# Optimization experiments

Measured on AMD Instinct MI355X. Metric: run time of the kernel, lower is better.

## Reference

```python
import jax, jax.numpy as jnp
import numpy as np

N, B, C_IN, C, E = 50000, 2, 64, 64, 800000


def _xavier(k, shape):
    bound = np.sqrt(6.0 / (shape[0] + shape[1]))
    return jax.random.uniform(k, shape, jnp.float32, -bound, bound)


def setup_inputs() -> dict:
    key = jax.random.key(0)
    ks = jax.random.split(key, 12)
    X = jax.random.normal(ks[0], (N, B, C_IN), jnp.float32)
    edge_index = jax.random.randint(ks[1], (2, E), 0, N, jnp.int64)
    edge_weight = jax.random.uniform(ks[2], (E,), jnp.float32)
    weight_n = _xavier(ks[3], (C_IN, C))
    weight_e = _xavier(ks[4], (1, C))
    query_w = _xavier(ks[5], (C, C))
    key_w = _xavier(ks[6], (C, C))
    # nn.Linear(3C, 1): store transposed weight [3C, 1] and bias [1]
    lb = 1.0 / np.sqrt(3 * C)
    att_w = jax.random.uniform(ks[7], (3 * C, 1), jnp.float32, -lb, lb)
    att_b = jax.random.uniform(ks[8], (1,), jnp.float32, -lb, lb)
    # nn.Linear(2C, C): store transposed weight [2C, C] and bias [C]
    lb2 = 1.0 / np.sqrt(2 * C)
    out_w = jax.random.uniform(ks[9], (2 * C, C), jnp.float32, -lb2, lb2)
    out_b = jax.random.uniform(ks[10], (C,), jnp.float32, -lb2, lb2)
    return {
        "X": X, "edge_index": edge_index, "edge_weight": edge_weight,
        "weight_n": weight_n, "weight_e": weight_e,
        "query_w": query_w, "key_w": key_w,
        "att_w": att_w, "att_b": att_b,
        "out_w": out_w, "out_b": out_b,
    }


def reference(X, edge_index, edge_weight, weight_n, weight_e,
              query_w, key_w, att_w, att_b, out_w, out_b):
    # node projection: [N, B, C]
    x = jnp.einsum('nbi,ic->nbc', X, weight_n)
    src, dst = edge_index[0], edge_index[1]  # x_j = x[src], x_i = x[dst]
    # edge embedding: [E, C]
    edge_emb = edge_weight[:, None] * weight_e[0][None, :]

    x_j = x[src]  # [E, B, C]
    x_i = x[dst]  # [E, B, C]
    q = jnp.einsum('ebc,cd->ebd', x_j, query_w)
    k = jnp.einsum('ebc,cd->ebd', x_i, key_w)
    # linear_att on concat([q, k, edge_emb]) == split matmul (avoids [E,B,3C] concat)
    wq, wk, we = att_w[:C], att_w[C:2 * C], att_w[2 * C:]
    att_logit = (q @ wq) + (k @ wk) + (edge_emb @ we)[:, None, :] + att_b  # [E, B, 1]
    att = jax.nn.sigmoid(att_logit)
    gate = jax.nn.sigmoid(edge_emb)[:, None, :]  # [E, 1, C]
    msg = att * x_j * gate  # [E, B, C]

    aggr = jax.ops.segment_sum(msg, dst, num_segments=N)  # [N, B, C]

    # linear_out(cat([x, aggr])) as split matmul
    upd = (jnp.einsum('nbc,cd->nbd', x, out_w[:C])
           + jnp.einsum('nbc,cd->nbd', aggr, out_w[C:]) + out_b)
    return x + upd
```

## Files before the change

### kernel.cpp

```cpp
#include <hip/hip_runtime.h>

#define NN 50000
#define BB 2
#define CC 64
#define EE 800000
#define RR (NN * BB)
#define K1BLK (RR / 32)
#define K2BLK (EE / 256)
#define NSCAN ((NN + 255) / 256)

typedef float f4_t __attribute__((ext_vector_type(4)));
typedef float f2_t __attribute__((ext_vector_type(2)));

#define LOG2E 1.44269504f

__device__ __forceinline__ float fsig_(float x) {
    return __builtin_amdgcn_rcpf(1.0f + __builtin_amdgcn_exp2f(x * -LOG2E));
}

__device__ __forceinline__ float bcast_(float v, int d) {
    return __uint_as_float(__builtin_amdgcn_readlane(__float_as_uint(v), d));
}

__global__ void k0_prep(const float* __restrict__ qw, const float* __restrict__ kw,
                        const float* __restrict__ we, const float* __restrict__ aw,
                        const float* __restrict__ wn, const float* __restrict__ ow,
                        float* __restrict__ prep, float* __restrict__ Wc) {
    int t = threadIdx.x;
    if (blockIdx.x == 0) {
        __shared__ float qv_s[64], kv_s[64];
        if (t < 64) {
            float sq = 0.f, sk = 0.f;
            for (int d = 0; d < 64; ++d) {
                sq = fmaf(qw[t * 64 + d], aw[d], sq);
                sk = fmaf(kw[t * 64 + d], aw[64 + d], sk);
            }
            qv_s[t] = sq; kv_s[t] = sk;
            prep[t] = sq; prep[64 + t] = sk;
            prep[320 + t] = -we[t] * LOG2E;
        }
        if (t == 128) {
            float se = 0.f;
            for (int i = 0; i < 64; ++i) se = fmaf(we[i], aw[128 + i], se);
            prep[128] = se;
        }
        __syncthreads();
        if (t < 64) {
            float s = 0.f;
            for (int c = 0; c < 64; ++c) s = fmaf(wn[t * 64 + c], qv_s[c], s);
            prep[192 + t] = s;
        } else if (t < 128) {
            int d = t - 64;
            float s = 0.f;
            for (int c = 0; c < 64; ++c) s = fmaf(wn[d * 64 + c], kv_s[c], s);
            prep[256 + d] = s;
        }
    } else {
        int idx = (blockIdx.x - 1) * 256 + t;
        int d = idx >> 6, c = idx & 63;
        float s = wn[d * 64 + c];
        for (int k = 0; k < 64; ++k) s = fmaf(wn[d * 64 + k], ow[k * 64 + c], s);
        Wc[idx] = s;
    }
}

__global__ void __launch_bounds__(256) k12(
        const float* __restrict__ X, const float* __restrict__ wn,
        const float* __restrict__ Wc, const float* __restrict__ out_b,
        const float* __restrict__ prep, const int* __restrict__ ei,
        float* __restrict__ x2f, float* __restrict__ y0,
        float* __restrict__ dq, float* __restrict__ dk,
        int* __restrict__ count) {
    int t = threadIdx.x;
    if (blockIdx.x < K2BLK) {
        int e = blockIdx.x * 256 + t;
        if (e < EE) atomicAdd(&count[ei[EE + e]], 1);
        return;
    }
    int wave = ((blockIdx.x - K2BLK) * 256 + t) >> 6;
    int lane = t & 63;
    int r0 = wave * 8;
    if (r0 >= RR) return;

    float xin[8];
    #pragma unroll
    for (int j = 0; j < 8; ++j) xin[j] = X[(r0 + j) * 64 + lane];

    float nq_l = prep[192 + lane];
    float nk_l = prep[256 + lane];

    float accx[8], accy[8];
    #pragma unroll
    for (int j = 0; j < 8; ++j) { accx[j] = 0.f; accy[j] = 0.f; }

    #pragma unroll 16
    for (int d = 0; d < 64; ++d) {
        float w0 = wn[d * 64 + lane];
        float wc = Wc[d * 64 + lane];
        #pragma unroll
        for (int j = 0; j < 8; ++j) {
            float s = bcast_(xin[j], d);
            accx[j] = fmaf(s, w0, accx[j]);
            accy[j] = fmaf(s, wc, accy[j]);
        }
    }

    float ob = out_b[lane];
    #pragma unroll
    for (int j = 0; j < 8; ++j) {
        int r = r0 + j;
        y0[r * 64 + lane] = accy[j] + ob;
        x2f[((r >> 1) * 64 + lane) * 2 + (r & 1)] = accx[j];
        float pq = xin[j] * nq_l;
        float pk = xin[j] * nk_l;
        #pragma unroll
        for (int o = 32; o > 0; o >>= 1) {
            pq += __shfl_xor(pq, o, 64);
            pk += __shfl_xor(pk, o, 64);
        }
        if (lane == j) { dq[r] = pq; dk[r] = pk; }
    }
}

__global__ void __launch_bounds__(256) k3a(const int* __restrict__ count,
                                           int* __restrict__ incl,
                                           int* __restrict__ bsum) {
    __shared__ int wsum[4];
    int t = threadIdx.x;
    int i = blockIdx.x * 256 + t;
    int v = (i < NN) ? count[i] : 0;
    int s = v;
    #pragma unroll
    for (int o = 1; o < 64; o <<= 1) {
        int u = __shfl_up(s, o, 64);
        if ((t & 63) >= o) s += u;
    }
    if ((t & 63) == 63) wsum[t >> 6] = s;
    __syncthreads();
    int add = 0;
    for (int w = 0; w < (t >> 6); ++w) add += wsum[w];
    s += add;
    if (i < NN) incl[i] = s;
    if (t == 255) bsum[blockIdx.x] = s;
}

__global__ void __launch_bounds__(256) k3b(const int* __restrict__ bsum,
                                           int* __restrict__ bscan) {
    __shared__ int wsum[4];
    int t = threadIdx.x;
    int v = (t < NSCAN) ? bsum[t] : 0;
    int s = v;
    #pragma unroll
    for (int o = 1; o < 64; o <<= 1) {
        int u = __shfl_up(s, o, 64);
        if ((t & 63) >= o) s += u;
    }
    if ((t & 63) == 63) wsum[t >> 6] = s;
    __syncthreads();
    int add = 0;
    for (int w = 0; w < (t >> 6); ++w) add += wsum[w];
    bscan[t] = s + add;
}

__global__ void __launch_bounds__(256) k3c(const int* __restrict__ count,
                                           const int* __restrict__ incl,
                                           const int* __restrict__ bscan,
                                           int* __restrict__ offs,
                                           int* __restrict__ cursor) {
    int t = threadIdx.x;
    int i = blockIdx.x * 256 + t;
    if (i < NN) {
        int base = blockIdx.x ? bscan[blockIdx.x - 1] : 0;
        int excl = base + incl[i] - count[i];
        offs[i] = excl;
        cursor[i] = excl;
    }
    if (i == 0) offs[NN] = EE;
}

__global__ void k4_scatter(const int* __restrict__ ei, const float* __restrict__ ew,
                           const float2* __restrict__ dq2, const float2* __restrict__ dk2,
                           const float* __restrict__ prep, const float* __restrict__ att_b,
                           int* __restrict__ cursor, f4_t* __restrict__ csr) {
    int e = blockIdx.x * blockDim.x + threadIdx.x;
    if (e >= EE) return;
    int src = ei[e], dst = ei[EE + e];
    float w = ew[e];
    float2 q = dq2[src];
    float2 k = dk2[dst];
    float esc = fmaf(w, prep[128], att_b[0]);
    float a0 = fsig_(q.x + k.x + esc);
    float a1 = fsig_(q.y + k.y + esc);
    int pos = atomicAdd(&cursor[dst], 1);
    f4_t rec = { __int_as_float(src), w, a0, a1 };
    __builtin_nontemporal_store(rec, &csr[pos]);
}

__global__ void __launch_bounds__(256) k5_aggr(
        const int* __restrict__ offs, const f4_t* __restrict__ csr,
        const f2_t* __restrict__ x2, const float* __restrict__ y0,
        const float* __restrict__ prep, const float* __restrict__ ow,
        float* __restrict__ out) {
    __shared__ float w1[4096];
    int t = threadIdx.x;
    #pragma unroll
    for (int j = 0; j < 16; ++j) w1[t + j * 256] = ow[4096 + t + j * 256];
    __syncthreads();

    int n = (blockIdx.x * 256 + t) >> 6;
    int lane = t & 63;
    if (n >= NN) return;

    float weL = prep[320 + lane];
    int s0 = offs[n], s1 = offs[n + 1];
    int cnt = s1 - s0;
    const f4_t* cp = csr + s0;

    float a0 = 0.f, a1 = 0.f;
    int i = 0;
    for (; i + 2 <= cnt; i += 2) {
        f4_t c0 = __builtin_nontemporal_load(cp + i);
        f4_t c1 = __builtin_nontemporal_load(cp + i + 1);
        f2_t xj0 = x2[__float_as_int(c0.x) * 64 + lane];
        f2_t xj1 = x2[__float_as_int(c1.x) * 64 + lane];
        float g0 = __builtin_amdgcn_rcpf(1.0f + __builtin_amdgcn_exp2f(c0.y * weL));
        float g1 = __builtin_amdgcn_rcpf(1.0f + __builtin_amdgcn_exp2f(c1.y * weL));
        a0 = fmaf(c0.z * g0, xj0.x, a0);
        a1 = fmaf(c0.w * g0, xj0.y, a1);
        a0 = fmaf(c1.z * g1, xj1.x, a0);
        a1 = fmaf(c1.w * g1, xj1.y, a1);
    }
    if (i < cnt) {
        f4_t c0 = __builtin_nontemporal_load(cp + i);
        f2_t xj0 = x2[__float_as_int(c0.x) * 64 + lane];
        float g0 = __builtin_amdgcn_rcpf(1.0f + __builtin_amdgcn_exp2f(c0.y * weL));
        a0 = fmaf(c0.z * g0, xj0.x, a0);
        a1 = fmaf(c0.w * g0, xj0.y, a1);
    }

    float o0 = __builtin_nontemporal_load(&y0[(2 * n) * 64 + lane]);
    float o1 = __builtin_nontemporal_load(&y0[(2 * n + 1) * 64 + lane]);
    #pragma unroll 16
    for (int d = 0; d < 64; ++d) {
        float wv = w1[d * 64 + lane];
        o0 = fmaf(bcast_(a0, d), wv, o0);
        o1 = fmaf(bcast_(a1, d), wv, o1);
    }
    __builtin_nontemporal_store(o0, &out[(2 * n) * 64 + lane]);
    __builtin_nontemporal_store(o1, &out[(2 * n + 1) * 64 + lane]);
}

extern "C" void kernel_launch(void* const* d_in, const int* in_sizes, int n_in,
                              void* d_out, int out_size, void* d_ws, size_t ws_size,
                              hipStream_t stream) {
    const float* X        = (const float*)d_in[0];
    const int*   ei       = (const int*)d_in[1];
    const float* ew       = (const float*)d_in[2];
    const float* weight_n = (const float*)d_in[3];
    const float* weight_e = (const float*)d_in[4];
    const float* query_w  = (const float*)d_in[5];
    const float* key_w    = (const float*)d_in[6];
    const float* att_w    = (const float*)d_in[7];
    const float* att_b    = (const float*)d_in[8];
    const float* out_w    = (const float*)d_in[9];
    const float* out_b    = (const float*)d_in[10];
    float* out = (float*)d_out;

    char* ws = (char*)d_ws;
    size_t off = 0;
    auto alloc = [&](size_t bytes) {
        char* p = ws + off;
        off += (bytes + 255) & ~(size_t)255;
        return p;
    };
    float*  x2f    = (float*)alloc(sizeof(float) * NN * CC * BB);
    float*  y0     = (float*)alloc(sizeof(float) * RR * CC);
    float*  dq     = (float*)alloc(sizeof(float) * RR);
    float*  dk     = (float*)alloc(sizeof(float) * RR);
    float*  prep   = (float*)alloc(sizeof(float) * 512);
    float*  Wc     = (float*)alloc(sizeof(float) * 4096);
    int*    count  = (int*)alloc(sizeof(int) * NN);
    int*    incl   = (int*)alloc(sizeof(int) * NN);
    int*    offs   = (int*)alloc(sizeof(int) * (NN + 1));
    int*    cursor = (int*)alloc(sizeof(int) * NN);
    int*    bsum   = (int*)alloc(sizeof(int) * 256);
    int*    bscan  = (int*)alloc(sizeof(int) * 256);
    f4_t*   csr    = (f4_t*)alloc(sizeof(f4_t) * EE);

    hipMemsetAsync(count, 0, sizeof(int) * NN, stream);

    hipLaunchKernelGGL(k0_prep, dim3(17), dim3(256), 0, stream,
                       query_w, key_w, weight_e, att_w, weight_n, out_w, prep, Wc);
    hipLaunchKernelGGL(k12, dim3(K1BLK + K2BLK), dim3(256), 0, stream,
                       X, weight_n, Wc, out_b, prep, ei, x2f, y0, dq, dk, count);
    hipLaunchKernelGGL(k3a, dim3(NSCAN), dim3(256), 0, stream,
                       count, incl, bsum);
    hipLaunchKernelGGL(k3b, dim3(1), dim3(256), 0, stream, bsum, bscan);
    hipLaunchKernelGGL(k3c, dim3(NSCAN), dim3(256), 0, stream,
                       count, incl, bscan, offs, cursor);
    hipLaunchKernelGGL(k4_scatter, dim3(K2BLK), dim3(256), 0, stream,
                       ei, ew, (const float2*)dq, (const float2*)dk, prep, att_b,
                       cursor, csr);
    hipLaunchKernelGGL(k5_aggr, dim3(NN / 4), dim3(256), 0, stream,
                       offs, csr, (const f2_t*)x2f, y0, prep, out_w, out);
}
```

Before: 316.3 us.

## Split aggregation and output matmul into separate kernels, unroll gather by four

The fused aggregate-plus-output-projection kernel is split in two. The aggregation kernel no longer stages a 16KB weight tile in LDS, which should raise occupancy for the latency-bound gather, and it unrolls the edge loop by four. A new k6 kernel does the 64x64 output matmul with each wave handling 8 rows. CSR records now hold the premultiplied src*64 index, offsets are made wave-uniform, and nontemporal hints are dropped on CSR traffic. The cost is an extra intermediate aggr buffer (about 25MB written and then read again) plus one more kernel launch.

```diff
diff --git a/kernel.cpp b/kernel.cpp
--- a/kernel.cpp
+++ b/kernel.cpp
@@ -192,62 +192,82 @@
     float a0 = fsig_(q.x + k.x + esc);
     float a1 = fsig_(q.y + k.y + esc);
     int pos = atomicAdd(&cursor[dst], 1);
-    f4_t rec = { __int_as_float(src), w, a0, a1 };
-    __builtin_nontemporal_store(rec, &csr[pos]);
+    f4_t rec = { __int_as_float(src * 64), w, a0, a1 };
+    csr[pos] = rec;
 }
 
 __global__ void __launch_bounds__(256) k5_aggr(
         const int* __restrict__ offs, const f4_t* __restrict__ csr,
-        const f2_t* __restrict__ x2, const float* __restrict__ y0,
-        const float* __restrict__ prep, const float* __restrict__ ow,
-        float* __restrict__ out) {
-    __shared__ float w1[4096];
-    int t = threadIdx.x;
-    #pragma unroll
-    for (int j = 0; j < 16; ++j) w1[t + j * 256] = ow[4096 + t + j * 256];
-    __syncthreads();
-
-    int n = (blockIdx.x * 256 + t) >> 6;
-    int lane = t & 63;
+        const f2_t* __restrict__ x2, const float* __restrict__ prep,
+        float* __restrict__ aggr) {
+    int n = (blockIdx.x * 256 + threadIdx.x) >> 6;
+    int lane = threadIdx.x & 63;
     if (n >= NN) return;
 
     float weL = prep[320 + lane];
-    int s0 = offs[n], s1 = offs[n + 1];
+    int s0 = __builtin_amdgcn_readfirstlane(offs[n]);
+    int s1 = __builtin_amdgcn_readfirstlane(offs[n + 1]);
     int cnt = s1 - s0;
     const f4_t* cp = csr + s0;
 
     float a0 = 0.f, a1 = 0.f;
     int i = 0;
-    for (; i + 2 <= cnt; i += 2) {
-        f4_t c0 = __builtin_nontemporal_load(cp + i);
-        f4_t c1 = __builtin_nontemporal_load(cp + i + 1);
-        f2_t xj0 = x2[__float_as_int(c0.x) * 64 + lane];
-        f2_t xj1 = x2[__float_as_int(c1.x) * 64 + lane];
+    for (; i + 4 <= cnt; i += 4) {
+        f4_t c0 = cp[i + 0];
+        f4_t c1 = cp[i + 1];
+        f4_t c2 = cp[i + 2];
+        f4_t c3 = cp[i + 3];
+        f2_t v0 = x2[__float_as_int(c0.x) + lane];
+        f2_t v1 = x2[__float_as_int(c1.x) + lane];
+        f2_t v2 = x2[__float_as_int(c2.x) + lane];
+        f2_t v3 = x2[__float_as_int(c3.x) + lane];
         float g0 = __builtin_amdgcn_rcpf(1.0f + __builtin_amdgcn_exp2f(c0.y * weL));
         float g1 = __builtin_amdgcn_rcpf(1.0f + __builtin_amdgcn_exp2f(c1.y * weL));
-        a0 = fmaf(c0.z * g0, xj0.x, a0);
-        a1 = fmaf(c0.w * g0, xj0.y, a1);
-        a0 = fmaf(c1.z * g1, xj1.x, a0);
-        a1 = fmaf(c1.w * g1, xj1.y, a1);
-    }
-    if (i < cnt) {
-        f4_t c0 = __builtin_nontemporal_load(cp + i);
-        f2_t xj0 = x2[__float_as_int(c0.x) * 64 + lane];
+        float g2 = __builtin_amdgcn_rcpf(1.0f + __builtin_amdgcn_exp2f(c2.y * weL));
+        float g3 = __builtin_amdgcn_rcpf(1.0f + __builtin_amdgcn_exp2f(c3.y * weL));
+        a0 = fmaf(c0.z * g0, v0.x, a0);  a1 = fmaf(c0.w * g0, v0.y, a1);
+        a0 = fmaf(c1.z * g1, v1.x, a0);  a1 = fmaf(c1.w * g1, v1.y, a1);
+        a0 = fmaf(c2.z * g2, v2.x, a0);  a1 = fmaf(c2.w * g2, v2.y, a1);
+        a0 = fmaf(c3.z * g3, v3.x, a0);  a1 = fmaf(c3.w * g3, v3.y, a1);
+    }
+    for (; i < cnt; ++i) {
+        f4_t c0 = cp[i];
+        f2_t v0 = x2[__float_as_int(c0.x) + lane];
         float g0 = __builtin_amdgcn_rcpf(1.0f + __builtin_amdgcn_exp2f(c0.y * weL));
-        a0 = fmaf(c0.z * g0, xj0.x, a0);
-        a1 = fmaf(c0.w * g0, xj0.y, a1);
-    }
-
-    float o0 = __builtin_nontemporal_load(&y0[(2 * n) * 64 + lane]);
-    float o1 = __builtin_nontemporal_load(&y0[(2 * n + 1) * 64 + lane]);
+        a0 = fmaf(c0.z * g0, v0.x, a0);
+        a1 = fmaf(c0.w * g0, v0.y, a1);
+    }
+
+    __builtin_nontemporal_store(a0, &aggr[(2 * n) * 64 + lane]);
+    __builtin_nontemporal_store(a1, &aggr[(2 * n + 1) * 64 + lane]);
+}
+
+__global__ void __launch_bounds__(256) k6_out(
+        const float* __restrict__ aggr, const float* __restrict__ y0,
+        const float* __restrict__ ow, float* __restrict__ out) {
+    int wave = (blockIdx.x * 256 + threadIdx.x) >> 6;
+    int lane = threadIdx.x & 63;
+    int r0 = wave * 8;
+    if (r0 >= RR) return;
+
+    float ain[8], acc[8];
+    #pragma unroll
+    for (int j = 0; j < 8; ++j) {
+        ain[j] = __builtin_nontemporal_load(&aggr[(r0 + j) * 64 + lane]);
+        acc[j] = __builtin_nontemporal_load(&y0[(r0 + j) * 64 + lane]);
+    }
+
     #pragma unroll 16
     for (int d = 0; d < 64; ++d) {
-        float wv = w1[d * 64 + lane];
-        o0 = fmaf(bcast_(a0, d), wv, o0);
-        o1 = fmaf(bcast_(a1, d), wv, o1);
-    }
-    __builtin_nontemporal_store(o0, &out[(2 * n) * 64 + lane]);
-    __builtin_nontemporal_store(o1, &out[(2 * n + 1) * 64 + lane]);
+        float w = ow[4096 + d * 64 + lane];
+        #pragma unroll
+        for (int j = 0; j < 8; ++j)
+            acc[j] = fmaf(bcast_(ain[j], d), w, acc[j]);
+    }
+
+    #pragma unroll
+    for (int j = 0; j < 8; ++j)
+        __builtin_nontemporal_store(acc[j], &out[(r0 + j) * 64 + lane]);
 }
 
 extern "C" void kernel_launch(void* const* d_in, const int* in_sizes, int n_in,
@@ -275,6 +295,7 @@
     };
     float*  x2f    = (float*)alloc(sizeof(float) * NN * CC * BB);
     float*  y0     = (float*)alloc(sizeof(float) * RR * CC);
+    float*  aggr   = (float*)alloc(sizeof(float) * RR * CC);
     float*  dq     = (float*)alloc(sizeof(float) * RR);
     float*  dk     = (float*)alloc(sizeof(float) * RR);
     float*  prep   = (float*)alloc(sizeof(float) * 512);
@@ -302,5 +323,7 @@
                        ei, ew, (const float2*)dq, (const float2*)dk, prep, att_b,
                        cursor, csr);
     hipLaunchKernelGGL(k5_aggr, dim3(NN / 4), dim3(256), 0, stream,
-                       offs, csr, (const f2_t*)x2f, y0, prep, out_w, out);
-}
+                       offs, csr, (const f2_t*)x2f, prep, aggr);
+    hipLaunchKernelGGL(k6_out, dim3(RR / 32), dim3(256), 0, stream,
+                       aggr, y0, out_w, out);
+}
```

After: 315.3 us. Within noise of the previous version (-0.3%).
